# Kernel tuning notes

Hardware: AMD Instinct MI355X
Metric: run time of the kernel (lower is better)

## Reference

```python
import jax, jax.numpy as jnp
import numpy as np

N = 100000
IN_C = 128
HID_C = 128
OUT_C = 128
E = 3200000


def setup_inputs() -> dict:
    key = jax.random.key(0)
    ks = jax.random.split(key, 8)
    x = jax.random.normal(ks[0], (N, IN_C), dtype=jnp.float32)
    edge_index = jax.random.randint(ks[1], (2, E), 0, N, dtype=jnp.int64)
    edge_weight = jnp.ones((E,), dtype=jnp.float32)
    s = 1.0 / np.sqrt(HID_C)
    W_conv = jax.random.uniform(ks[2], (HID_C, IN_C), jnp.float32, -s, s)
    b_conv = jnp.zeros((HID_C,), dtype=jnp.float32)
    W_fc = jax.random.uniform(ks[3], (HID_C, HID_C), jnp.float32, -s, s)
    b_fc = jax.random.uniform(ks[4], (HID_C,), jnp.float32, -s, s)
    W_fc2 = jax.random.uniform(ks[5], (OUT_C, HID_C), jnp.float32, -s, s)
    b_fc2 = jax.random.uniform(ks[6], (OUT_C,), jnp.float32, -s, s)
    return {"x": x, "edge_index": edge_index, "edge_weight": edge_weight,
            "W_conv": W_conv, "b_conv": b_conv, "W_fc": W_fc, "b_fc": b_fc,
            "W_fc2": W_fc2, "b_fc2": b_fc2}


def _gcn_conv(x, edge_index, edge_weight, W_conv, b_conv):
    n = x.shape[0]
    # add self-loops with weight 1 (PyG GCNConv default)
    loop = jnp.arange(n, dtype=edge_index.dtype)
    src = jnp.concatenate([edge_index[0], loop])
    dst = jnp.concatenate([edge_index[1], loop])
    ew = jnp.concatenate([edge_weight, jnp.ones((n,), dtype=edge_weight.dtype)])
    # symmetric normalization: deg^-1/2[src] * w * deg^-1/2[dst]
    deg = jax.ops.segment_sum(ew, dst, num_segments=n)
    dinv = jnp.where(deg > 0, jax.lax.rsqrt(jnp.where(deg > 0, deg, 1.0)), 0.0)
    norm = dinv[src] * ew * dinv[dst]  # [E+N]
    h = x @ W_conv.T                   # [N, hid], bias-free linear first
    msg = h[src] * norm[:, None]       # gather + scale
    agg = jax.ops.segment_sum(msg, dst, num_segments=n)  # scatter-add
    return agg + b_conv


def reference(x, edge_index, edge_weight, W_conv, b_conv, W_fc, b_fc, W_fc2, b_fc2):
    h = _gcn_conv(x, edge_index, edge_weight, W_conv, b_conv)
    h = jax.nn.relu(h)
    h = jax.nn.relu(h @ W_fc.T + b_fc)
    return h @ W_fc2.T + b_fc2
```

## Files before the change

### kernel.cpp

```cpp
#include <hip/hip_runtime.h>

typedef short bf16x8 __attribute__((ext_vector_type(8)));
typedef short bf16x4 __attribute__((ext_vector_type(4)));
typedef float f32x4 __attribute__((ext_vector_type(4)));
typedef float f32x2 __attribute__((ext_vector_type(2)));

#define PS 64
#define PMAX 2048
#define CAPP 2432
#define NB 256

__device__ __forceinline__ unsigned short f2bf(float f) {
    unsigned int u = __float_as_uint(f);
    u = (u + 0x7FFFu + ((u >> 16) & 1u)) >> 16;
    return (unsigned short)u;
}

__global__ __launch_bounds__(1024) void scat_k(const int* __restrict__ ei,
                                               const float* __restrict__ ew,
                                               int* __restrict__ partCnt,
                                               int2* __restrict__ regions,
                                               int E, int P, int EPB) {
    __shared__ int cntl[PMAX];
    __shared__ int basel[PMAX];
    const int b = blockIdx.x, tid = threadIdx.x;
    for (int i = tid; i < P; i += 1024) cntl[i] = 0;
    __syncthreads();
    const int s = b * EPB, e = min(E, s + EPB);
    for (int i = s + tid; i < e; i += 1024)
        atomicAdd(&cntl[ei[E + i] >> 6], 1);
    __syncthreads();
    for (int p = tid; p < P; p += 1024) {
        int c = cntl[p];
        basel[p] = p * CAPP + (c ? atomicAdd(&partCnt[p], c) : 0);
        cntl[p] = 0;
    }
    __syncthreads();
    for (int i = s + tid; i < e; i += 1024) {
        int src = ei[i];
        int dst = ei[E + i];
        float w = ew[i];
        int p = dst >> 6, dl = dst & 63;
        int lidx = atomicAdd(&cntl[p], 1);
        int pos = basel[p] + lidx;
        if (pos < (p + 1) * CAPP)
            regions[pos] = make_int2(src | (dl << 24), __float_as_int(w));
    }
}

__global__ __launch_bounds__(256) void dgemm1_k(const float* __restrict__ x,
                                                const float* __restrict__ Wc,
                                                const int* __restrict__ partCnt,
                                                const int2* __restrict__ regions,
                                                float* __restrict__ dinv,
                                                int* __restrict__ nodeOff,
                                                unsigned short* __restrict__ h,
                                                int M, int P) {
    __shared__ __align__(16) unsigned short Wl[128 * 136];
    __shared__ float degl[256];
    __shared__ int cl[256];
    const int tid = threadIdx.x;
    degl[tid] = 0.f; cl[tid] = 0;

#pragma unroll
    for (int i = 0; i < 16; ++i) {
        int e4 = i * 256 + tid;
        float4 v = ((const float4*)Wc)[e4];
        int e = e4 * 4, r = e >> 7, cc = e & 127;
        unsigned short* pp = &Wl[r * 136 + cc];
        pp[0] = f2bf(v.x); pp[1] = f2bf(v.y); pp[2] = f2bf(v.z); pp[3] = f2bf(v.w);
    }
    __syncthreads();

#pragma unroll
    for (int q = 0; q < 4; ++q) {
        int p = blockIdx.x * 4 + q;
        if (p < P) {
            const int cnt = min(partCnt[p], CAPP);
            const int2* reg = regions + (size_t)p * CAPP;
            for (int i = tid; i < cnt; i += 256) {
                int2 r = reg[i];
                int dl = q * 64 + ((r.x >> 24) & 63);
                atomicAdd(&cl[dl], 1);
                atomicAdd(&degl[dl], __int_as_float(r.y));
            }
        }
    }
    __syncthreads();
    {
        int lane = tid & 63;
        int cn = cl[tid];
        int v = cn;
#pragma unroll
        for (int off = 1; off < 64; off <<= 1) {
            int u = __shfl_up(v, off, 64);
            if (lane >= off) v += u;
        }
        int node = blockIdx.x * 256 + tid;
        float d = rsqrtf(1.0f + degl[tid]);
        if (node < M) { nodeOff[node] = v - cn; dinv[node] = d; }
        degl[tid] = d;
    }
    __syncthreads();

    const int wave = tid >> 6, lane = tid & 63;
    const int m = lane & 15, quad = lane >> 4;

#pragma unroll
    for (int t = 0; t < 4; ++t) {
        const int tileBase = blockIdx.x * 256 + t * 64;
        if (tileBase >= M) break;
        const int rowBase = tileBase + wave * 16;
        int arow = rowBase + m;
        int arowc = arow < M ? arow : (M - 1);

        bf16x8 afrag[4];
        const float* pa = x + (size_t)arowc * 128 + quad * 8;
#pragma unroll
        for (int kc = 0; kc < 4; ++kc) {
            float4 v0 = *(const float4*)(pa + kc * 32);
            float4 v1 = *(const float4*)(pa + kc * 32 + 4);
            bf16x8 f;
            f[0] = (short)f2bf(v0.x); f[1] = (short)f2bf(v0.y);
            f[2] = (short)f2bf(v0.z); f[3] = (short)f2bf(v0.w);
            f[4] = (short)f2bf(v1.x); f[5] = (short)f2bf(v1.y);
            f[6] = (short)f2bf(v1.z); f[7] = (short)f2bf(v1.w);
            afrag[kc] = f;
        }

        float dv[4];
#pragma unroll
        for (int r = 0; r < 4; ++r)
            dv[r] = degl[t * 64 + wave * 16 + quad * 4 + r];

#pragma unroll
        for (int nt = 0; nt < 8; ++nt) {
            f32x4 acc = {0.f, 0.f, 0.f, 0.f};
            const unsigned short* wb = &Wl[(nt * 16 + m) * 136 + quad * 8];
#pragma unroll
            for (int kc = 0; kc < 4; ++kc) {
                bf16x8 bfrag = *(const bf16x8*)(wb + kc * 32);
                acc = __builtin_amdgcn_mfma_f32_16x16x32_bf16(afrag[kc], bfrag, acc, 0, 0, 0);
            }
            const int col = nt * 16 + m;
#pragma unroll
            for (int r = 0; r < 4; ++r) {
                int row = rowBase + quad * 4 + r;
                if (row < M)
                    h[((size_t)(col >> 6) * M + row) * 64 + (col & 63)] = f2bf(acc[r] * dv[r]);
            }
        }
    }
}

__global__ __launch_bounds__(256) void aggF_k(const int* __restrict__ partCnt,
                                              const int* __restrict__ nodeOff,
                                              const int2* __restrict__ regions,
                                              const unsigned short* __restrict__ h,
                                              const float* __restrict__ dinv,
                                              const float* __restrict__ bconv,
                                              unsigned short* __restrict__ h2, int N) {
    __shared__ __align__(16) int2 stag[CAPP];
    __shared__ int cstart[PS + 1];
    __shared__ int wcur[PS];
    const int p = blockIdx.x, tid = threadIdx.x;
    const int cnt = min(partCnt[p], CAPP);
    const int2* reg = regions + (size_t)p * CAPP;

    if (tid < PS) {
        int node = p * PS + tid;
        int o = (node < N) ? nodeOff[node] : cnt;
        cstart[tid] = o;
        wcur[tid] = o;
    } else if (tid == PS) {
        cstart[PS] = cnt;
    }
    __syncthreads();
    for (int i = tid; i < cnt; i += 256) {
        int2 r = reg[i];
        int pos = atomicAdd(&wcur[(r.x >> 24) & 63], 1);
        stag[pos] = make_int2((r.x & 0xFFFFFF) << 7, r.y);
    }
    __syncthreads();

    const int wave = tid >> 6, lane = tid & 63;
    const int g = lane >> 4;
    const int c4 = (lane & 15) * 4;
    const int c4b = c4 * 2;

#define ACC2(q, w) {                                                        \
        unsigned ux = (unsigned)(q).x, uy = (unsigned)(q).y;                \
        f32x2 ww; ww[0] = (w); ww[1] = (w);                                 \
        f32x2 v01, v23;                                                     \
        v01[0] = __uint_as_float(ux << 16);                                 \
        v01[1] = __uint_as_float(ux & 0xFFFF0000u);                         \
        v23[0] = __uint_as_float(uy << 16);                                 \
        v23[1] = __uint_as_float(uy & 0xFFFF0000u);                         \
        a01 = v01 * ww + a01; a23 = v23 * ww + a23; }

#pragma unroll
    for (int hh = 0; hh < 2; ++hh) {
        const char* hb = (const char*)h + ((size_t)hh * (size_t)N << 7);
        for (int nl = wave; nl < PS; nl += 4) {
            int n = p * PS + nl;
            if (n >= N) continue;
            const int s = cstart[nl], e = cstart[nl + 1];
            f32x2 a01 = {0.f, 0.f}, a23 = {0.f, 0.f};
            int j = s;
            const int e32 = s + ((e - s) & ~31);
            for (; j < e32; j += 32) {
                int2 r0 = stag[j + g];
                int2 r1 = stag[j + 4 + g];
                int2 r2 = stag[j + 8 + g];
                int2 r3 = stag[j + 12 + g];
                int2 r4 = stag[j + 16 + g];
                int2 r5 = stag[j + 20 + g];
                int2 r6 = stag[j + 24 + g];
                int2 r7 = stag[j + 28 + g];
                int2 q0 = *(const int2*)(hb + ((unsigned)r0.x + c4b));
                int2 q1 = *(const int2*)(hb + ((unsigned)r1.x + c4b));
                int2 q2 = *(const int2*)(hb + ((unsigned)r2.x + c4b));
                int2 q3 = *(const int2*)(hb + ((unsigned)r3.x + c4b));
                int2 q4 = *(const int2*)(hb + ((unsigned)r4.x + c4b));
                int2 q5 = *(const int2*)(hb + ((unsigned)r5.x + c4b));
                int2 q6 = *(const int2*)(hb + ((unsigned)r6.x + c4b));
                int2 q7 = *(const int2*)(hb + ((unsigned)r7.x + c4b));
                ACC2(q0, __int_as_float(r0.y));
                ACC2(q1, __int_as_float(r1.y));
                ACC2(q2, __int_as_float(r2.y));
                ACC2(q3, __int_as_float(r3.y));
                ACC2(q4, __int_as_float(r4.y));
                ACC2(q5, __int_as_float(r5.y));
                ACC2(q6, __int_as_float(r6.y));
                ACC2(q7, __int_as_float(r7.y));
            }
            const int e16 = s + ((e - s) & ~15);
            for (; j < e16; j += 16) {
                int2 r0 = stag[j + g];
                int2 r1 = stag[j + 4 + g];
                int2 r2 = stag[j + 8 + g];
                int2 r3 = stag[j + 12 + g];
                int2 q0 = *(const int2*)(hb + ((unsigned)r0.x + c4b));
                int2 q1 = *(const int2*)(hb + ((unsigned)r1.x + c4b));
                int2 q2 = *(const int2*)(hb + ((unsigned)r2.x + c4b));
                int2 q3 = *(const int2*)(hb + ((unsigned)r3.x + c4b));
                ACC2(q0, __int_as_float(r0.y));
                ACC2(q1, __int_as_float(r1.y));
                ACC2(q2, __int_as_float(r2.y));
                ACC2(q3, __int_as_float(r3.y));
            }
            for (; j < e; j += 8) {
                int j0 = j + g, j1 = j + 4 + g;
                int2 r0 = stag[j0 < e ? j0 : s];
                int2 r1 = stag[j1 < e ? j1 : s];
                float w0 = (j0 < e) ? __int_as_float(r0.y) : 0.f;
                float w1 = (j1 < e) ? __int_as_float(r1.y) : 0.f;
                int2 q0 = *(const int2*)(hb + ((unsigned)r0.x + c4b));
                int2 q1 = *(const int2*)(hb + ((unsigned)r1.x + c4b));
                ACC2(q0, w0);
                ACC2(q1, w1);
            }
            float acc[4] = {a01[0], a01[1], a23[0], a23[1]};
#pragma unroll
            for (int k = 0; k < 4; ++k) {
                float v = acc[k];
                v += __shfl_xor(v, 16, 64);
                v += __shfl_xor(v, 32, 64);
                acc[k] = v;
            }
            if (g == 0) {
                float di = dinv[n];
                int2 qs = *(const int2*)(hb + (((size_t)(unsigned)n << 7) + c4b));
                float4 b = *(const float4*)(bconv + hh * 64 + c4);
                unsigned ux = (unsigned)qs.x, uy = (unsigned)qs.y;
                bf16x4 o;
                o[0] = (short)f2bf(fmaxf(di * (acc[0] + __uint_as_float(ux << 16)) + b.x, 0.f));
                o[1] = (short)f2bf(fmaxf(di * (acc[1] + __uint_as_float(ux & 0xFFFF0000u)) + b.y, 0.f));
                o[2] = (short)f2bf(fmaxf(di * (acc[2] + __uint_as_float(uy << 16)) + b.z, 0.f));
                o[3] = (short)f2bf(fmaxf(di * (acc[3] + __uint_as_float(uy & 0xFFFF0000u)) + b.w, 0.f));
                *(bf16x4*)(h2 + (size_t)n * 128 + hh * 64 + c4) = o;
            }
        }
    }
#undef ACC2
}

__global__ __launch_bounds__(256) void gemm23_k(const unsigned short* __restrict__ h2,
                                                const float* __restrict__ Wf,
                                                const float* __restrict__ bfc,
                                                const float* __restrict__ W2,
                                                const float* __restrict__ b2,
                                                float* __restrict__ out, int M) {
    __shared__ __align__(16) unsigned short Wl[128 * 136];
    __shared__ __align__(16) unsigned short Tl[64 * 136];
    const int tid = threadIdx.x;

#pragma unroll
    for (int i = 0; i < 16; ++i) {
        int e4 = i * 256 + tid;
        float4 v = ((const float4*)Wf)[e4];
        int e = e4 * 4, r = e >> 7, cc = e & 127;
        unsigned short* pp = &Wl[r * 136 + cc];
        pp[0] = f2bf(v.x); pp[1] = f2bf(v.y); pp[2] = f2bf(v.z); pp[3] = f2bf(v.w);
    }
    __syncthreads();

    const int wave = tid >> 6, lane = tid & 63;
    const int m = lane & 15, quad = lane >> 4;
    const int rowBase = blockIdx.x * 64 + wave * 16;
    int arow = rowBase + m;
    int arowc = arow < M ? arow : (M - 1);

    bf16x8 afrag[4];
    {
        const unsigned short* pa = h2 + (size_t)arowc * 128 + quad * 8;
#pragma unroll
        for (int kc = 0; kc < 4; ++kc)
            afrag[kc] = *(const bf16x8*)(pa + kc * 32);
    }

#pragma unroll
    for (int nt = 0; nt < 8; ++nt) {
        f32x4 acc = {0.f, 0.f, 0.f, 0.f};
        const unsigned short* wb = &Wl[(nt * 16 + m) * 136 + quad * 8];
#pragma unroll
        for (int kc = 0; kc < 4; ++kc) {
            bf16x8 bfrag = *(const bf16x8*)(wb + kc * 32);
            acc = __builtin_amdgcn_mfma_f32_16x16x32_bf16(afrag[kc], bfrag, acc, 0, 0, 0);
        }
        const int col = nt * 16 + m;
        float bv = bfc[col];
#pragma unroll
        for (int r = 0; r < 4; ++r) {
            int rowl = wave * 16 + quad * 4 + r;
            Tl[rowl * 136 + col] = f2bf(fmaxf(acc[r] + bv, 0.f));
        }
    }
    __syncthreads();

#pragma unroll
    for (int i = 0; i < 16; ++i) {
        int e4 = i * 256 + tid;
        float4 v = ((const float4*)W2)[e4];
        int e = e4 * 4, r = e >> 7, cc = e & 127;
        unsigned short* pp = &Wl[r * 136 + cc];
        pp[0] = f2bf(v.x); pp[1] = f2bf(v.y); pp[2] = f2bf(v.z); pp[3] = f2bf(v.w);
    }
    __syncthreads();

    bf16x8 afrag2[4];
    {
        const unsigned short* pa = &Tl[(wave * 16 + m) * 136 + quad * 8];
#pragma unroll
        for (int kc = 0; kc < 4; ++kc)
            afrag2[kc] = *(const bf16x8*)(pa + kc * 32);
    }
#pragma unroll
    for (int nt = 0; nt < 8; ++nt) {
        f32x4 acc = {0.f, 0.f, 0.f, 0.f};
        const unsigned short* wb = &Wl[(nt * 16 + m) * 136 + quad * 8];
#pragma unroll
        for (int kc = 0; kc < 4; ++kc) {
            bf16x8 bfrag = *(const bf16x8*)(wb + kc * 32);
            acc = __builtin_amdgcn_mfma_f32_16x16x32_bf16(afrag2[kc], bfrag, acc, 0, 0, 0);
        }
        const int col = nt * 16 + m;
        float bv = b2[col];
#pragma unroll
        for (int r = 0; r < 4; ++r) {
            int row = rowBase + quad * 4 + r;
            if (row < M)
                out[(size_t)row * 128 + col] = acc[r] + bv;
        }
    }
}

extern "C" void kernel_launch(void* const* d_in, const int* in_sizes, int n_in,
                              void* d_out, int out_size, void* d_ws, size_t ws_size,
                              hipStream_t stream) {
    const float* x  = (const float*)d_in[0];
    const int* ei   = (const int*)d_in[1];
    const float* ew = (const float*)d_in[2];
    const float* Wc = (const float*)d_in[3];
    const float* bc = (const float*)d_in[4];
    const float* Wf = (const float*)d_in[5];
    const float* bf = (const float*)d_in[6];
    const float* W2 = (const float*)d_in[7];
    const float* b2 = (const float*)d_in[8];
    float* out = (float*)d_out;

    const int N = in_sizes[0] / 128;
    const int E = in_sizes[2];
    const int P = (N + PS - 1) / PS;

    auto align256 = [](size_t v) { return (v + 255) & ~(size_t)255; };
    char* ws = (char*)d_ws;
    size_t off = 0;
    float* dinv  = (float*)(ws + off); off += align256((size_t)N * 4);
    int* nodeOff = (int*)(ws + off);   off += align256((size_t)N * 4);
    int* partCnt = (int*)(ws + off);   off += align256((size_t)P * 4);
    unsigned short* h  = (unsigned short*)(ws + off); off += (size_t)N * 256;
    unsigned short* h2 = (unsigned short*)(ws + off);

    int2* regions = (int2*)out;

    const int EPB = (E + NB - 1) / NB;

    hipMemsetAsync(partCnt, 0, (size_t)P * 4, stream);
    scat_k<<<NB, 1024, 0, stream>>>(ei, ew, partCnt, regions, E, P, EPB);
    dgemm1_k<<<(N + 255) / 256, 256, 0, stream>>>(x, Wc, partCnt, regions, dinv, nodeOff, h, N, P);
    aggF_k<<<P, 256, 0, stream>>>(partCnt, nodeOff, regions, h, dinv, bc, h2, N);
    gemm23_k<<<(N + 63) / 64, 256, 0, stream>>>(h2, Wf, bf, W2, b2, out, N);
}
```

Before: 374.3 us.

## Halve destination partition size and pre-convert weights to bf16 once

Destination partitions shrink from 64 to 32 nodes, so there are twice as many partitions (and aggregation blocks), with smaller staging capacity per partition. The aim is better load balance and occupancy in the aggregation kernel, since its shared staging buffer gets smaller. Separately, the first 12 blocks of the scatter kernel convert the three weight matrices to bf16 once, so each GEMM block copies ready-made bf16 data instead of redoing the fp32-to-bf16 conversion. The costs are more partitions for the scatter pass's shared counters and atomics, and a tighter per-partition capacity that could overflow on skewed degree distributions.

After: 362.3 us. 3.2% less time.

```diff
diff --git a/kernel.cpp b/kernel.cpp
--- a/kernel.cpp
+++ b/kernel.cpp
@@ -5,9 +5,9 @@
 typedef float f32x4 __attribute__((ext_vector_type(4)));
 typedef float f32x2 __attribute__((ext_vector_type(2)));
 
-#define PS 64
-#define PMAX 2048
-#define CAPP 2432
+#define PS 32
+#define PMAX 4096
+#define CAPP 1312
 #define NB 256
 
 __device__ __forceinline__ unsigned short f2bf(float f) {
@@ -20,15 +20,33 @@
                                                const float* __restrict__ ew,
                                                int* __restrict__ partCnt,
                                                int2* __restrict__ regions,
+                                               const float* __restrict__ Wc,
+                                               const float* __restrict__ Wf,
+                                               const float* __restrict__ W2,
+                                               unsigned short* __restrict__ wcb,
+                                               unsigned short* __restrict__ wfb,
+                                               unsigned short* __restrict__ w2b,
                                                int E, int P, int EPB) {
     __shared__ int cntl[PMAX];
     __shared__ int basel[PMAX];
     const int b = blockIdx.x, tid = threadIdx.x;
+
+    if (b < 12) {
+        int t = (b << 10) | tid;
+        int a = t >> 12, idx = t & 4095;
+        const float4* s4 = (const float4*)(a == 0 ? Wc : (a == 1 ? Wf : W2));
+        unsigned short* dw = (a == 0 ? wcb : (a == 1 ? wfb : w2b));
+        float4 v = s4[idx];
+        ushort4 o;
+        o.x = f2bf(v.x); o.y = f2bf(v.y); o.z = f2bf(v.z); o.w = f2bf(v.w);
+        *(ushort4*)(dw + idx * 4) = o;
+    }
+
     for (int i = tid; i < P; i += 1024) cntl[i] = 0;
     __syncthreads();
     const int s = b * EPB, e = min(E, s + EPB);
     for (int i = s + tid; i < e; i += 1024)
-        atomicAdd(&cntl[ei[E + i] >> 6], 1);
+        atomicAdd(&cntl[ei[E + i] >> 5], 1);
     __syncthreads();
     for (int p = tid; p < P; p += 1024) {
         int c = cntl[p];
@@ -40,7 +58,7 @@
         int src = ei[i];
         int dst = ei[E + i];
         float w = ew[i];
-        int p = dst >> 6, dl = dst & 63;
+        int p = dst >> 5, dl = dst & 31;
         int lidx = atomicAdd(&cntl[p], 1);
         int pos = basel[p] + lidx;
         if (pos < (p + 1) * CAPP)
@@ -49,7 +67,7 @@
 }
 
 __global__ __launch_bounds__(256) void dgemm1_k(const float* __restrict__ x,
-                                                const float* __restrict__ Wc,
+                                                const unsigned short* __restrict__ Wcb,
                                                 const int* __restrict__ partCnt,
                                                 const int2* __restrict__ regions,
                                                 float* __restrict__ dinv,
@@ -63,24 +81,22 @@
     degl[tid] = 0.f; cl[tid] = 0;
 
 #pragma unroll
-    for (int i = 0; i < 16; ++i) {
-        int e4 = i * 256 + tid;
-        float4 v = ((const float4*)Wc)[e4];
-        int e = e4 * 4, r = e >> 7, cc = e & 127;
-        unsigned short* pp = &Wl[r * 136 + cc];
-        pp[0] = f2bf(v.x); pp[1] = f2bf(v.y); pp[2] = f2bf(v.z); pp[3] = f2bf(v.w);
-    }
-    __syncthreads();
-
-#pragma unroll
-    for (int q = 0; q < 4; ++q) {
-        int p = blockIdx.x * 4 + q;
+    for (int i = 0; i < 8; ++i) {
+        int c = i * 256 + tid;
+        int r = c >> 4, col = (c & 15) * 8;
+        *(bf16x8*)&Wl[r * 136 + col] = *(const bf16x8*)(Wcb + c * 8);
+    }
+    __syncthreads();
+
+#pragma unroll
+    for (int q = 0; q < 8; ++q) {
+        int p = blockIdx.x * 8 + q;
         if (p < P) {
             const int cnt = min(partCnt[p], CAPP);
             const int2* reg = regions + (size_t)p * CAPP;
             for (int i = tid; i < cnt; i += 256) {
                 int2 r = reg[i];
-                int dl = q * 64 + ((r.x >> 24) & 63);
+                int dl = q * 32 + ((r.x >> 24) & 31);
                 atomicAdd(&cl[dl], 1);
                 atomicAdd(&degl[dl], __int_as_float(r.y));
             }
@@ -88,13 +104,13 @@
     }
     __syncthreads();
     {
-        int lane = tid & 63;
+        int l32 = tid & 31;
         int cn = cl[tid];
         int v = cn;
 #pragma unroll
-        for (int off = 1; off < 64; off <<= 1) {
-            int u = __shfl_up(v, off, 64);
-            if (lane >= off) v += u;
+        for (int off = 1; off < 32; off <<= 1) {
+            int u = __shfl_up(v, off, 32);
+            if (l32 >= off) v += u;
         }
         int node = blockIdx.x * 256 + tid;
         float d = rsqrtf(1.0f + degl[tid]);
@@ -178,7 +194,7 @@
     __syncthreads();
     for (int i = tid; i < cnt; i += 256) {
         int2 r = reg[i];
-        int pos = atomicAdd(&wcur[(r.x >> 24) & 63], 1);
+        int pos = atomicAdd(&wcur[(r.x >> 24) & 31], 1);
         stag[pos] = make_int2((r.x & 0xFFFFFF) << 7, r.y);
     }
     __syncthreads();
@@ -286,9 +302,9 @@
 }
 
 __global__ __launch_bounds__(256) void gemm23_k(const unsigned short* __restrict__ h2,
-                                                const float* __restrict__ Wf,
+                                                const unsigned short* __restrict__ Wfb,
                                                 const float* __restrict__ bfc,
-                                                const float* __restrict__ W2,
+                                                const unsigned short* __restrict__ W2b,
                                                 const float* __restrict__ b2,
                                                 float* __restrict__ out, int M) {
     __shared__ __align__(16) unsigned short Wl[128 * 136];
@@ -296,12 +312,10 @@
     const int tid = threadIdx.x;
 
 #pragma unroll
-    for (int i = 0; i < 16; ++i) {
-        int e4 = i * 256 + tid;
-        float4 v = ((const float4*)Wf)[e4];
-        int e = e4 * 4, r = e >> 7, cc = e & 127;
-        unsigned short* pp = &Wl[r * 136 + cc];
-        pp[0] = f2bf(v.x); pp[1] = f2bf(v.y); pp[2] = f2bf(v.z); pp[3] = f2bf(v.w);
+    for (int i = 0; i < 8; ++i) {
+        int c = i * 256 + tid;
+        int r = c >> 4, col = (c & 15) * 8;
+        *(bf16x8*)&Wl[r * 136 + col] = *(const bf16x8*)(Wfb + c * 8);
     }
     __syncthreads();
 
@@ -339,12 +353,10 @@
     __syncthreads();
 
 #pragma unroll
-    for (int i = 0; i < 16; ++i) {
-        int e4 = i * 256 + tid;
-        float4 v = ((const float4*)W2)[e4];
-        int e = e4 * 4, r = e >> 7, cc = e & 127;
-        unsigned short* pp = &Wl[r * 136 + cc];
-        pp[0] = f2bf(v.x); pp[1] = f2bf(v.y); pp[2] = f2bf(v.z); pp[3] = f2bf(v.w);
+    for (int i = 0; i < 8; ++i) {
+        int c = i * 256 + tid;
+        int r = c >> 4, col = (c & 15) * 8;
+        *(bf16x8*)&Wl[r * 136 + col] = *(const bf16x8*)(W2b + c * 8);
     }
     __syncthreads();
 
@@ -399,6 +411,9 @@
     float* dinv  = (float*)(ws + off); off += align256((size_t)N * 4);
     int* nodeOff = (int*)(ws + off);   off += align256((size_t)N * 4);
     int* partCnt = (int*)(ws + off);   off += align256((size_t)P * 4);
+    unsigned short* wcb = (unsigned short*)(ws + off); off += align256(16384 * 2);
+    unsigned short* wfb = (unsigned short*)(ws + off); off += align256(16384 * 2);
+    unsigned short* w2b = (unsigned short*)(ws + off); off += align256(16384 * 2);
     unsigned short* h  = (unsigned short*)(ws + off); off += (size_t)N * 256;
     unsigned short* h2 = (unsigned short*)(ws + off);
 
@@ -407,8 +422,8 @@
     const int EPB = (E + NB - 1) / NB;
 
     hipMemsetAsync(partCnt, 0, (size_t)P * 4, stream);
-    scat_k<<<NB, 1024, 0, stream>>>(ei, ew, partCnt, regions, E, P, EPB);
-    dgemm1_k<<<(N + 255) / 256, 256, 0, stream>>>(x, Wc, partCnt, regions, dinv, nodeOff, h, N, P);
+    scat_k<<<NB, 1024, 0, stream>>>(ei, ew, partCnt, regions, Wc, Wf, W2, wcb, wfb, w2b, E, P, EPB);
+    dgemm1_k<<<(N + 255) / 256, 256, 0, stream>>>(x, wcb, partCnt, regions, dinv, nodeOff, h, N, P);
     aggF_k<<<P, 256, 0, stream>>>(partCnt, nodeOff, regions, h, dinv, bc, h2, N);
-    gemm23_k<<<(N + 63) / 64, 256, 0, stream>>>(h2, Wf, bf, W2, b2, out, N);
-}
+    gemm23_k<<<(N + 63) / 64, 256, 0, stream>>>(h2, wfb, bf, w2b, b2, out, N);
+}
```
